# Performance work log

Hardware: AMD Instinct MI355X
Metric: run time of the kernel (lower is better)

Reference implementation:

```python
import jax, jax.numpy as jnp
import numpy as np

TOP_K = 2


def setup_inputs() -> dict:
    key = jax.random.key(0)
    k1, k2, k3 = jax.random.split(key, 3)
    inp = jax.random.normal(k1, (16384, 2048), dtype=jnp.float32)
    W = jax.random.normal(k2, (64, 2048), dtype=jnp.float32) * 0.02
    b = jax.random.normal(k3, (64,), dtype=jnp.float32) * 0.02
    return {"inp": inp, "W": W, "b": b}


def reference(inp, W, b):
    # gate logits: [tokens, num_expert]
    gate = jnp.einsum("td,ed->te", inp, W) + b
    # top-k over experts (lax.top_k returns sorted; torch used sorted=False,
    # so results match up to a per-token permutation of the k slots)
    top_val, top_idx = jax.lax.top_k(gate, TOP_K)  # [tokens, k]
    gate_score = jax.nn.softmax(top_val, axis=-1)[:, None, :]  # [tokens, 1, k]
    gate_top_k_idx = top_idx.reshape(-1)  # [tokens * k]
    return (gate_top_k_idx, gate_score)
```

## Files before the change

kernel.cpp:

```cpp
#include <hip/hip_runtime.h>
#include <math.h>


#define KDIM 2048
#define NEXP 64
#define BK 32
#define TM 64
#define LDSS 68

__global__ __launch_bounds__(256) void gate_topk_kernel(
    const float* __restrict__ inp,
    const float* __restrict__ W,
    const float* __restrict__ bias,
    float* __restrict__ out,
    int tokens)
{
    __shared__ float As[BK][LDSS];
    __shared__ float Ws[BK][LDSS];

    const int tid = threadIdx.x;
    const int tx  = tid & 15;
    const int ty  = tid >> 4;
    const int tokBase = blockIdx.x * TM;

    const int lrow = tid >> 3;
    const int lcol = (tid & 7) << 2;

    const float* aPtr0 = inp + (size_t)(tokBase + lrow)      * KDIM + lcol;
    const float* aPtr1 = inp + (size_t)(tokBase + lrow + 32) * KDIM + lcol;
    const float* wPtr0 = W   + (size_t)lrow        * KDIM + lcol;
    const float* wPtr1 = W   + (size_t)(lrow + 32) * KDIM + lcol;

    float4 aReg0, aReg1, wReg0, wReg1;
    aReg0 = *(const float4*)(aPtr0);
    aReg1 = *(const float4*)(aPtr1);
    wReg0 = *(const float4*)(wPtr0);
    wReg1 = *(const float4*)(wPtr1);

    float acc[4][4];
    #pragma unroll
    for (int r = 0; r < 4; ++r)
        #pragma unroll
        for (int c = 0; c < 4; ++c) acc[r][c] = 0.0f;

    const int NT = KDIM / BK;
    for (int kt = 0; kt < NT; ++kt) {
        __syncthreads();
        #pragma unroll
        for (int c = 0; c < 4; ++c) {
            As[lcol + c][lrow]      = ((const float*)&aReg0)[c];
            As[lcol + c][lrow + 32] = ((const float*)&aReg1)[c];
            Ws[lcol + c][lrow]      = ((const float*)&wReg0)[c];
            Ws[lcol + c][lrow + 32] = ((const float*)&wReg1)[c];
        }
        __syncthreads();
        if (kt + 1 < NT) {
            const int off = (kt + 1) * BK;
            aReg0 = *(const float4*)(aPtr0 + off);
            aReg1 = *(const float4*)(aPtr1 + off);
            wReg0 = *(const float4*)(wPtr0 + off);
            wReg1 = *(const float4*)(wPtr1 + off);
        }
        #pragma unroll 8
        for (int kk = 0; kk < BK; ++kk) {
            const float4 av = *(const float4*)&As[kk][ty << 2];
            const float4 wv = *(const float4*)&Ws[kk][tx << 2];
            const float a[4] = {av.x, av.y, av.z, av.w};
            const float w[4] = {wv.x, wv.y, wv.z, wv.w};
            #pragma unroll
            for (int r = 0; r < 4; ++r)
                #pragma unroll
                for (int c = 0; c < 4; ++c)
                    acc[r][c] = fmaf(a[r], w[c], acc[r][c]);
        }
    }

    const int eBase = tx << 2;
    float bv[4];
    #pragma unroll
    for (int c = 0; c < 4; ++c) bv[c] = bias[eBase + c];

    const int scoreOff = tokens * 2;

    #pragma unroll
    for (int r = 0; r < 4; ++r) {
        float v1 = acc[r][0] + bv[0]; int i1 = eBase;
        float v2 = -INFINITY;         int i2 = -1;
        #pragma unroll
        for (int c = 1; c < 4; ++c) {
            const float vv = acc[r][c] + bv[c];
            const int   ii = eBase + c;
            if (vv > v1)      { v2 = v1; i2 = i1; v1 = vv; i1 = ii; }
            else if (vv > v2) { v2 = vv; i2 = ii; }
        }
        #pragma unroll
        for (int m = 1; m <= 8; m <<= 1) {
            const float ov1 = __shfl_xor(v1, m);
            const int   oi1 = __shfl_xor(i1, m);
            const float ov2 = __shfl_xor(v2, m);
            const int   oi2 = __shfl_xor(i2, m);
            const bool aw = (v1 > ov1) || (v1 == ov1 && i1 < oi1);
            const float nv1 = aw ? v1  : ov1;  const int ni1 = aw ? i1  : oi1;
            const float lv  = aw ? ov1 : v1;   const int li  = aw ? oi1 : i1;
            const float sv  = aw ? v2  : ov2;  const int si  = aw ? i2  : oi2;
            const bool sw = (sv > lv) || (sv == lv && si < li);
            v1 = nv1; i1 = ni1;
            v2 = sw ? sv : lv; i2 = sw ? si : li;
        }
        if (tx == 0) {
            const int token = tokBase + (ty << 2) + r;
            const float e2 = expf(v2 - v1);
            const float denom = 1.0f + e2;
            const float p1 = 1.0f / denom;
            const float p2 = e2 / denom;
            out[2 * token]     = (float)i1;
            out[2 * token + 1] = (float)i2;
            out[scoreOff + 2 * token]     = p1;
            out[scoreOff + 2 * token + 1] = p2;
        }
    }
}

extern "C" void kernel_launch(void* const* d_in, const int* in_sizes, int n_in,
                              void* d_out, int out_size, void* d_ws, size_t ws_size,
                              hipStream_t stream) {
    const float* inp  = (const float*)d_in[0];
    const float* W    = (const float*)d_in[1];
    const float* bias = (const float*)d_in[2];
    float* out = (float*)d_out;

    const int tokens = in_sizes[0] / KDIM;
    const int grid = tokens / TM;

    gate_topk_kernel<<<grid, 256, 0, stream>>>(inp, W, bias, out, tokens);
}
```

Before: 239.8 us.

## Split K dimension across blocks and reduce partials in a second kernel

Result: faster. 218.2 us (-9.0%).

```diff
diff --git a/kernel.cpp b/kernel.cpp
--- a/kernel.cpp
+++ b/kernel.cpp
@@ -4,16 +4,15 @@
 
 #define KDIM 2048
 #define NEXP 64
+#define TM 64
 #define BK 32
-#define TM 64
 #define LDSS 68
 
-__global__ __launch_bounds__(256) void gate_topk_kernel(
+__global__ __launch_bounds__(256) void gate_partial_kernel(
     const float* __restrict__ inp,
     const float* __restrict__ W,
-    const float* __restrict__ bias,
-    float* __restrict__ out,
-    int tokens)
+    float* __restrict__ partial,
+    int tokens, int kPerSplit)
 {
     __shared__ float As[BK][LDSS];
     __shared__ float Ws[BK][LDSS];
@@ -22,20 +21,21 @@
     const int tx  = tid & 15;
     const int ty  = tid >> 4;
     const int tokBase = blockIdx.x * TM;
+    const int split   = blockIdx.y;
+    const int k0      = split * kPerSplit;
 
     const int lrow = tid >> 3;
     const int lcol = (tid & 7) << 2;
 
-    const float* aPtr0 = inp + (size_t)(tokBase + lrow)      * KDIM + lcol;
-    const float* aPtr1 = inp + (size_t)(tokBase + lrow + 32) * KDIM + lcol;
-    const float* wPtr0 = W   + (size_t)lrow        * KDIM + lcol;
-    const float* wPtr1 = W   + (size_t)(lrow + 32) * KDIM + lcol;
+    const float* aPtr0 = inp + (size_t)(tokBase + lrow)      * KDIM + k0 + lcol;
+    const float* aPtr1 = inp + (size_t)(tokBase + lrow + 32) * KDIM + k0 + lcol;
+    const float* wPtr0 = W   + (size_t)lrow        * KDIM + k0 + lcol;
+    const float* wPtr1 = W   + (size_t)(lrow + 32) * KDIM + k0 + lcol;
 
-    float4 aReg0, aReg1, wReg0, wReg1;
-    aReg0 = *(const float4*)(aPtr0);
-    aReg1 = *(const float4*)(aPtr1);
-    wReg0 = *(const float4*)(wPtr0);
-    wReg1 = *(const float4*)(wPtr1);
+    float4 aReg0 = *(const float4*)(aPtr0);
+    float4 aReg1 = *(const float4*)(aPtr1);
+    float4 wReg0 = *(const float4*)(wPtr0);
+    float4 wReg1 = *(const float4*)(wPtr1);
 
     float acc[4][4];
     #pragma unroll
@@ -43,7 +43,7 @@
         #pragma unroll
         for (int c = 0; c < 4; ++c) acc[r][c] = 0.0f;
 
-    const int NT = KDIM / BK;
+    const int NT = kPerSplit / BK;
     for (int kt = 0; kt < NT; ++kt) {
         __syncthreads();
         #pragma unroll
@@ -76,48 +76,64 @@
     }
 
     const int eBase = tx << 2;
-    float bv[4];
-    #pragma unroll
-    for (int c = 0; c < 4; ++c) bv[c] = bias[eBase + c];
-
-    const int scoreOff = tokens * 2;
-
     #pragma unroll
     for (int r = 0; r < 4; ++r) {
-        float v1 = acc[r][0] + bv[0]; int i1 = eBase;
-        float v2 = -INFINITY;         int i2 = -1;
-        #pragma unroll
-        for (int c = 1; c < 4; ++c) {
-            const float vv = acc[r][c] + bv[c];
-            const int   ii = eBase + c;
-            if (vv > v1)      { v2 = v1; i2 = i1; v1 = vv; i1 = ii; }
-            else if (vv > v2) { v2 = vv; i2 = ii; }
-        }
-        #pragma unroll
-        for (int m = 1; m <= 8; m <<= 1) {
-            const float ov1 = __shfl_xor(v1, m);
-            const int   oi1 = __shfl_xor(i1, m);
-            const float ov2 = __shfl_xor(v2, m);
-            const int   oi2 = __shfl_xor(i2, m);
-            const bool aw = (v1 > ov1) || (v1 == ov1 && i1 < oi1);
-            const float nv1 = aw ? v1  : ov1;  const int ni1 = aw ? i1  : oi1;
-            const float lv  = aw ? ov1 : v1;   const int li  = aw ? oi1 : i1;
-            const float sv  = aw ? v2  : ov2;  const int si  = aw ? i2  : oi2;
-            const bool sw = (sv > lv) || (sv == lv && si < li);
-            v1 = nv1; i1 = ni1;
-            v2 = sw ? sv : lv; i2 = sw ? si : li;
-        }
-        if (tx == 0) {
-            const int token = tokBase + (ty << 2) + r;
-            const float e2 = expf(v2 - v1);
-            const float denom = 1.0f + e2;
-            const float p1 = 1.0f / denom;
-            const float p2 = e2 / denom;
-            out[2 * token]     = (float)i1;
-            out[2 * token + 1] = (float)i2;
-            out[scoreOff + 2 * token]     = p1;
-            out[scoreOff + 2 * token + 1] = p2;
-        }
+        const int token = tokBase + (ty << 2) + r;
+        float4 v = make_float4(acc[r][0], acc[r][1], acc[r][2], acc[r][3]);
+        *(float4*)&partial[((size_t)split * tokens + token) * NEXP + eBase] = v;
+    }
+}
+
+__global__ __launch_bounds__(256) void reduce_topk_kernel(
+    const float* __restrict__ partial,
+    const float* __restrict__ bias,
+    float* __restrict__ out,
+    int tokens, int S)
+{
+    const int tid = threadIdx.x;
+    const int tx  = tid & 15;
+    const int ty  = tid >> 4;
+    const int token = blockIdx.x * 16 + ty;
+    const int eBase = tx << 2;
+
+    float4 v = make_float4(0.f, 0.f, 0.f, 0.f);
+    for (int s = 0; s < S; ++s) {
+        const float4 p = *(const float4*)&partial[((size_t)s * tokens + token) * NEXP + eBase];
+        v.x += p.x; v.y += p.y; v.z += p.z; v.w += p.w;
+    }
+    const float4 bv = *(const float4*)&bias[eBase];
+    float g[4] = { v.x + bv.x, v.y + bv.y, v.z + bv.z, v.w + bv.w };
+
+    float v1 = g[0]; int i1 = eBase;
+    float v2 = -INFINITY; int i2 = -1;
+    #pragma unroll
+    for (int c = 1; c < 4; ++c) {
+        const float vv = g[c];
+        const int   ii = eBase + c;
+        if (vv > v1)      { v2 = v1; i2 = i1; v1 = vv; i1 = ii; }
+        else if (vv > v2) { v2 = vv; i2 = ii; }
+    }
+    #pragma unroll
+    for (int m = 1; m <= 8; m <<= 1) {
+        const float ov1 = __shfl_xor(v1, m);
+        const int   oi1 = __shfl_xor(i1, m);
+        const float ov2 = __shfl_xor(v2, m);
+        const int   oi2 = __shfl_xor(i2, m);
+        const bool aw = (v1 > ov1) || (v1 == ov1 && i1 < oi1);
+        const float nv1 = aw ? v1  : ov1;  const int ni1 = aw ? i1  : oi1;
+        const float lv  = aw ? ov1 : v1;   const int li  = aw ? oi1 : i1;
+        const float sv  = aw ? v2  : ov2;  const int si  = aw ? i2  : oi2;
+        const bool sw = (sv > lv) || (sv == lv && si < li);
+        v1 = nv1; i1 = ni1;
+        v2 = sw ? sv : lv; i2 = sw ? si : li;
+    }
+    if (tx == 0) {
+        const float e2 = expf(v2 - v1);
+        const float denom = 1.0f + e2;
+        out[2 * token]     = (float)i1;
+        out[2 * token + 1] = (float)i2;
+        out[tokens * 2 + 2 * token]     = 1.0f / denom;
+        out[tokens * 2 + 2 * token + 1] = e2 / denom;
     }
 }
 
@@ -128,9 +144,15 @@
     const float* W    = (const float*)d_in[1];
     const float* bias = (const float*)d_in[2];
     float* out = (float*)d_out;
+    float* partial = (float*)d_ws;
 
     const int tokens = in_sizes[0] / KDIM;
-    const int grid = tokens / TM;
 
-    gate_topk_kernel<<<grid, 256, 0, stream>>>(inp, W, bias, out, tokens);
+    int S = 4;
+    while (S > 1 && (size_t)S * tokens * NEXP * sizeof(float) > ws_size) S >>= 1;
+    const int kPerSplit = KDIM / S;
+
+    dim3 grid(tokens / TM, S);
+    gate_partial_kernel<<<grid, 256, 0, stream>>>(inp, W, partial, tokens, kPerSplit);
+    reduce_topk_kernel<<<tokens / 16, 256, 0, stream>>>(partial, bias, out, tokens, S);
 }
```
